# Kernel optimization log

Hardware: AMD Instinct MI355X
Metric: run time of the kernel (lower is better)

The kernel has to match this reference:

```python
import jax, jax.numpy as jnp
import numpy as np
import math

NUM_HEADS = 16
D_MODEL = 1024
B, T = 1, 4096


def setup_inputs() -> dict:
    key = jax.random.key(0)
    kx, kq, kk, kv, ko = jax.random.split(key, 5)
    s = 1.0 / math.sqrt(D_MODEL)
    return {
        "x": jax.random.normal(kx, (B, T, D_MODEL), dtype=jnp.float32),
        "Wq": jax.random.normal(kq, (D_MODEL, D_MODEL), dtype=jnp.float32) * s,
        "Wk": jax.random.normal(kk, (D_MODEL, D_MODEL), dtype=jnp.float32) * s,
        "Wv": jax.random.normal(kv, (D_MODEL, D_MODEL), dtype=jnp.float32) * s,
        "Wo": jax.random.normal(ko, (D_MODEL, D_MODEL), dtype=jnp.float32) * s,
    }


def reference(x, Wq, Wk, Wv, Wo):
    # x: (B, T, D); weights stored torch-Linear style: y = x @ W.T
    Bx, Tx, D = x.shape
    H = NUM_HEADS
    dk = D // H
    q = (x @ Wq.T).reshape(Bx, Tx, H, dk)  # (B,T,H,dk)
    k = (x @ Wk.T).reshape(Bx, Tx, H, dk)
    v = (x @ Wv.T).reshape(Bx, Tx, H, dk)
    # scores: (B,H,T,T), scaled dot-product
    scores = jnp.einsum("bthd,bshd->bhts", q, k) / math.sqrt(dk)
    causal_mask = jnp.triu(jnp.ones((Tx, Tx), dtype=bool), k=1)  # True above diag
    scores = jnp.where(causal_mask, jnp.float32(-jnp.inf), scores).astype(jnp.float32)
    attn = jax.nn.softmax(scores, axis=-1)  # fp32 softmax, as in the torch module
    out = jnp.einsum("bhts,bshd->bthd", attn, v).reshape(Bx, Tx, D)
    return out @ Wo.T
```

## Files before the change

kernel.cpp:

```cpp
#include <hip/hip_runtime.h>
#include <hip/hip_bf16.h>
#include <math.h>

typedef __attribute__((ext_vector_type(8)))  __bf16 bf16x8;
typedef __attribute__((ext_vector_type(4)))  __bf16 bf16x4;
typedef __attribute__((ext_vector_type(4)))  float  f32x4;
typedef __attribute__((ext_vector_type(16))) float  f32x16;

static constexpr int T_SEQ = 4096;
static constexpr int DM    = 1024;
static constexpr int NH    = 16;
static constexpr float QSCALE = 0.125f * 1.44269504088896340736f;

__device__ __forceinline__ void gload16(const void* g, void* l) {
    __builtin_amdgcn_global_load_lds(
        (const __attribute__((address_space(1))) unsigned int*)g,
        (__attribute__((address_space(3))) unsigned int*)l,
        16, 0, 0);
}

__device__ __forceinline__ unsigned cvtpk_bf16(float a, float b) {
    unsigned r;
    asm("v_cvt_pk_bf16_f32 %0, %1, %2" : "=v"(r) : "v"(a), "v"(b));
    return r;
}
__device__ __forceinline__ void permswap(unsigned& x, unsigned& y) {
    asm("v_permlane32_swap_b32 %0, %1" : "+v"(x), "+v"(y));
}
__device__ __forceinline__ float xhalf_max(float v) {
    union { float f; unsigned u; } a, b;
    a.f = v; b.f = v;
    asm volatile("" : "+v"(b.u));
    permswap(a.u, b.u);
    return fmaxf(a.f, b.f);
}
__device__ __forceinline__ float xhalf_sum(float v) {
    union { float f; unsigned u; } a, b;
    a.f = v; b.f = v;
    asm volatile("" : "+v"(b.u));
    permswap(a.u, b.u);
    return a.f + b.f;
}

__global__ __launch_bounds__(256)
void cvt_bf16(const float* __restrict__ in, __bf16* __restrict__ out, int n4) {
    int i = blockIdx.x * blockDim.x + threadIdx.x;
    if (i >= n4) return;
    float4 v = ((const float4*)in)[i];
    bf16x4 o;
    o[0] = (__bf16)v.x; o[1] = (__bf16)v.y; o[2] = (__bf16)v.z; o[3] = (__bf16)v.w;
    ((bf16x4*)out)[i] = o;
}

__global__ __launch_bounds__(256)
void cvt4_bf16(const float* __restrict__ a0, const float* __restrict__ a1,
               const float* __restrict__ a2, const float* __restrict__ a3,
               __bf16* __restrict__ o0, __bf16* __restrict__ o1,
               __bf16* __restrict__ o2, __bf16* __restrict__ o3, int n4) {
    int i = blockIdx.x * blockDim.x + threadIdx.x;
    if (i >= n4) return;
    const float* in = blockIdx.y == 0 ? a0 : blockIdx.y == 1 ? a1 : blockIdx.y == 2 ? a2 : a3;
    __bf16* out     = blockIdx.y == 0 ? o0 : blockIdx.y == 1 ? o1 : blockIdx.y == 2 ? o2 : o3;
    float4 v = ((const float4*)in)[i];
    bf16x4 o;
    o[0] = (__bf16)v.x; o[1] = (__bf16)v.y; o[2] = (__bf16)v.z; o[3] = (__bf16)v.w;
    ((bf16x4*)out)[i] = o;
}

template<bool OUT_BF16>
__device__ __forceinline__ void gemm_body(const __bf16* __restrict__ A,
                                          const __bf16* __restrict__ B,
                                          void* __restrict__ Cout,
                                          int N, int K, float scale,
                                          int bx, int by) {
    __shared__ __align__(16) __bf16 Al[128 * 64];
    __shared__ __align__(16) __bf16 Bl[128 * 64];
    const int tid  = threadIdx.x;
    const int lane = tid & 63;
    const int wid  = tid >> 6;
    const int wr   = wid >> 1, wc = wid & 1;
    const int m0   = by * 128, n0 = bx * 128;
    const int r    = lane & 15, g = lane >> 4;

    f32x4 acc[4][4];
    const f32x4 z4 = {0.f, 0.f, 0.f, 0.f};
    #pragma unroll
    for (int i = 0; i < 4; ++i)
        #pragma unroll
        for (int j = 0; j < 4; ++j) acc[i][j] = z4;

    for (int kt = 0; kt < K; kt += 64) {
        __syncthreads();
        #pragma unroll
        for (int p = 0; p < 4; ++p) {
            int u    = p * 256 + tid;
            int row  = u >> 3;
            int col8 = (u & 7) ^ (row & 7);
            gload16(A + (size_t)(m0 + row) * K + kt + col8 * 8,
                    (char*)Al + (p * 256 + wid * 64) * 16);
            gload16(B + (size_t)(n0 + row) * K + kt + col8 * 8,
                    (char*)Bl + (p * 256 + wid * 64) * 16);
        }
        __syncthreads();
        __builtin_amdgcn_s_setprio(1);
        #pragma unroll
        for (int kk = 0; kk < 2; ++kk) {
            bf16x8 af[4], bfr[4];
            #pragma unroll
            for (int mi = 0; mi < 4; ++mi)
                af[mi] = *(const bf16x8*)&Al[(wr * 64 + mi * 16 + r) * 64 + (((kk * 4 + g) ^ (r & 7)) * 8)];
            #pragma unroll
            for (int nj = 0; nj < 4; ++nj)
                bfr[nj] = *(const bf16x8*)&Bl[(wc * 64 + nj * 16 + r) * 64 + (((kk * 4 + g) ^ (r & 7)) * 8)];
            #pragma unroll
            for (int mi = 0; mi < 4; ++mi)
                #pragma unroll
                for (int nj = 0; nj < 4; ++nj)
                    acc[mi][nj] = __builtin_amdgcn_mfma_f32_16x16x32_bf16(af[mi], bfr[nj], acc[mi][nj], 0, 0, 0);
        }
        __builtin_amdgcn_s_setprio(0);
    }
    #pragma unroll
    for (int mi = 0; mi < 4; ++mi)
        #pragma unroll
        for (int nj = 0; nj < 4; ++nj)
            #pragma unroll
            for (int j = 0; j < 4; ++j) {
                int row = m0 + wr * 64 + mi * 16 + g * 4 + j;
                int col = n0 + wc * 64 + nj * 16 + r;
                float v = acc[mi][nj][j] * scale;
                if (OUT_BF16) ((__bf16*)Cout)[(size_t)row * N + col] = (__bf16)v;
                else          ((float*)Cout)[(size_t)row * N + col]  = v;
            }
}

__global__ __launch_bounds__(256)
void gemm_qkv(const __bf16* __restrict__ A,
              const __bf16* __restrict__ W0, const __bf16* __restrict__ W1,
              const __bf16* __restrict__ W2,
              __bf16* __restrict__ O0, __bf16* __restrict__ O1, __bf16* __restrict__ O2) {
    const int z = blockIdx.z;
    const __bf16* B = z == 0 ? W0 : (z == 1 ? W1 : W2);
    __bf16*       C = z == 0 ? O0 : (z == 1 ? O1 : O2);
    float scale = z == 0 ? QSCALE : 1.0f;
    gemm_body<true>(A, B, C, DM, DM, scale, blockIdx.x, blockIdx.y);
}

__global__ __launch_bounds__(256)
void gemm_out(const __bf16* __restrict__ A, const __bf16* __restrict__ B,
              float* __restrict__ C) {
    gemm_body<false>(A, B, C, DM, DM, 1.0f, blockIdx.x, blockIdx.y);
}

__global__ __launch_bounds__(256)
void vtrans(const __bf16* __restrict__ V, __bf16* __restrict__ Vt) {
    __shared__ __bf16 tl[64][72];
    const int tid = threadIdx.x;
    const int t0  = blockIdx.x * 64;
    const int h   = blockIdx.y;
    #pragma unroll
    for (int p = 0; p < 2; ++p) {
        int c = p * 256 + tid, row = c >> 3, col8 = c & 7;
        *(bf16x8*)&tl[row][col8 * 8] =
            *(const bf16x8*)(V + (size_t)(t0 + row) * DM + h * 64 + col8 * 8);
    }
    __syncthreads();
    #pragma unroll
    for (int p = 0; p < 2; ++p) {
        int c = p * 256 + tid, d = c >> 3, tc8 = c & 7;
        bf16x8 o;
        #pragma unroll
        for (int e = 0; e < 8; ++e) o[e] = tl[tc8 * 8 + e][d];
        *(bf16x8*)(Vt + (size_t)(h * 64 + d) * T_SEQ + t0 + tc8 * 8) = o;
    }
}

__global__ __launch_bounds__(128)
void attn_fwd(const __bf16* __restrict__ Q, const __bf16* __restrict__ Kp,
              const __bf16* __restrict__ Vt, __bf16* __restrict__ O)
{
    __shared__ __align__(16) __bf16 Kl[2][64 * 64];
    __shared__ __align__(16) __bf16 Vl[2][64 * 64];
    const int tid  = threadIdx.x;
    const int lane = tid & 63, wid = tid >> 6;
    const int l31  = lane & 31;
    const int hi   = lane >> 5;
    const int h    = blockIdx.x;
    const int u_   = blockIdx.y & 15, j_ = blockIdx.y >> 4;
    const int qb   = j_ == 0 ? u_ : j_ == 1 ? 31 - u_ : j_ == 2 ? 32 + u_ : 63 - u_;
    const int qw   = qb * 64 + wid * 32;
    const int qg   = qw + l31;

    bf16x8 qf[4];
    #pragma unroll
    for (int kd0 = 0; kd0 < 4; ++kd0)
        qf[kd0] = *(const bf16x8*)(Q + (size_t)qg * DM + h * 64 + kd0 * 16 + hi * 8);

    float m_i = -1e30f, l_i = 0.f;
    f32x16 oacc[2];
    #pragma unroll
    for (int d = 0; d < 2; ++d)
        #pragma unroll
        for (int e = 0; e < 16; ++e) oacc[d][e] = 0.f;

    const int nt = qb + 1;

    auto stage_lds = [&](int t, int buf) {
        #pragma unroll
        for (int p = 0; p < 4; ++p) {
            int u    = p * 128 + tid;
            int row  = u >> 3;
            int col8 = (u & 7) ^ (row & 7);
            gload16(Kp + (size_t)(t * 64 + row) * DM + h * 64 + col8 * 8,
                    (char*)&Kl[buf][0] + (p * 128 + wid * 64) * 16);
            gload16(Vt + (size_t)(h * 64 + row) * T_SEQ + t * 64 + col8 * 8,
                    (char*)&Vl[buf][0] + (p * 128 + wid * 64) * 16);
        }
    };
    stage_lds(0, 0);
    if (nt > 1) stage_lds(1, 1);
    __syncthreads();

    auto qk = [&](f32x16* sdst, int buf) {
        #pragma unroll
        for (int ksub = 0; ksub < 2; ++ksub) {
            const int row = ksub * 32 + l31;
            f32x16 a;
            #pragma unroll
            for (int e = 0; e < 16; ++e) a[e] = 0.f;
            #pragma unroll
            for (int kd0 = 0; kd0 < 4; ++kd0) {
                bf16x8 kf = *(const bf16x8*)
                    &Kl[buf][(row << 6) + ((((kd0 << 1) + hi) ^ (row & 7)) << 3)];
                a = __builtin_amdgcn_mfma_f32_32x32x16_bf16(kf, qf[kd0], a, 0, 0, 0);
            }
            sdst[ksub] = a;
        }
    };
    auto mask_sf = [&](f32x16* s, int t) {
        const int kb = (t << 6) + 4 * hi;
        #pragma unroll
        for (int ksub = 0; ksub < 2; ++ksub)
            #pragma unroll
            for (int e = 0; e < 16; ++e) {
                int k = kb + ksub * 32 + ((e & 3) + 8 * (e >> 2));
                if (k > qg) s[ksub][e] = -1e30f;
            }
    };

    f32x16 sf[2], sfn[2];
    qk(sf, 0);
    if (qb == 0) mask_sf(sf, 0);

    bf16x8 kreg[4], vreg[4];
    for (int t = 0; t < nt; ++t) {
        const int cur = t & 1;
        const bool have_next  = (t + 1 < nt);
        const bool have_next2 = (t + 2 < nt);
        if (have_next2) {
            const int t2 = t + 2;
            #pragma unroll
            for (int p = 0; p < 4; ++p) {
                int u   = p * 128 + tid;
                int row = u >> 3;
                int c   = u & 7;
                kreg[p] = *(const bf16x8*)(Kp + (size_t)(t2 * 64 + row) * DM + h * 64 + c * 8);
                vreg[p] = *(const bf16x8*)(Vt + (size_t)(h * 64 + row) * T_SEQ + t2 * 64 + c * 8);
            }
        }
        __builtin_amdgcn_s_setprio(1);
        if (have_next) {
            qk(sfn, cur ^ 1);
            if (t + 1 == qb) mask_sf(sfn, t + 1);
        }
        __builtin_amdgcn_s_setprio(0);
        float pm;
        {
            float t0[8];
            #pragma unroll
            for (int e = 0; e < 8; ++e)
                t0[e] = fmaxf(fmaxf(sf[0][e], sf[0][e + 8]), fmaxf(sf[1][e], sf[1][e + 8]));
            #pragma unroll
            for (int s = 4; s > 0; s >>= 1)
                #pragma unroll
                for (int e = 0; e < s; ++e) t0[e] = fmaxf(t0[e], t0[e + s]);
            pm = xhalf_max(t0[0]);
        }
        if (pm > m_i + 8.f) {
            float al = exp2f(m_i - pm);
            m_i = pm;
            l_i *= al;
            #pragma unroll
            for (int d = 0; d < 2; ++d)
                #pragma unroll
                for (int e = 0; e < 16; ++e) oacc[d][e] *= al;
        }
        float p[32];
        #pragma unroll
        for (int i = 0; i < 32; ++i)
            p[i] = exp2f(sf[i >> 4][i & 15] - m_i);
        {
            float s0[8];
            #pragma unroll
            for (int e = 0; e < 8; ++e)
                s0[e] = (p[e] + p[e + 8]) + (p[e + 16] + p[e + 24]);
            #pragma unroll
            for (int s = 4; s > 0; s >>= 1)
                #pragma unroll
                for (int e = 0; e < s; ++e) s0[e] += s0[e + s];
            l_i += xhalf_sum(s0[0]);
        }
        __builtin_amdgcn_s_setprio(1);
        #pragma unroll
        for (int ks = 0; ks < 4; ++ks) {
            unsigned w0 = cvtpk_bf16(p[8 * ks + 0], p[8 * ks + 1]);
            unsigned w1 = cvtpk_bf16(p[8 * ks + 2], p[8 * ks + 3]);
            unsigned w2 = cvtpk_bf16(p[8 * ks + 4], p[8 * ks + 5]);
            unsigned w3 = cvtpk_bf16(p[8 * ks + 6], p[8 * ks + 7]);
            permswap(w0, w2);
            permswap(w1, w3);
            union { unsigned u[4]; bf16x8 v; } pu;
            pu.u[0] = w0; pu.u[1] = w1; pu.u[2] = w2; pu.u[3] = w3;
            #pragma unroll
            for (int dsub = 0; dsub < 2; ++dsub) {
                const int row = dsub * 32 + l31;
                bf16x8 vt = *(const bf16x8*)
                    &Vl[cur][(row << 6) + ((((ks << 1) + hi) ^ (row & 7)) << 3)];
                oacc[dsub] = __builtin_amdgcn_mfma_f32_32x32x16_bf16(vt, pu.v, oacc[dsub], 0, 0, 0);
            }
        }
        __builtin_amdgcn_s_setprio(0);
        if (have_next2) {
            __syncthreads();
            #pragma unroll
            for (int p = 0; p < 4; ++p) {
                int u   = p * 128 + tid;
                int row = u >> 3;
                int c   = u & 7;
                *(bf16x8*)&Kl[cur][(row << 6) + ((c ^ (row & 7)) << 3)] = kreg[p];
                *(bf16x8*)&Vl[cur][(row << 6) + ((c ^ (row & 7)) << 3)] = vreg[p];
            }
            __syncthreads();
        }
        if (have_next) {
            sf[0] = sfn[0];
            sf[1] = sfn[1];
        }
    }
    __syncthreads();
    __bf16* ow = &Kl[0][0] + wid * 2048;
    const float invl = 1.f / l_i;
    #pragma unroll
    for (int dsub = 0; dsub < 2; ++dsub)
        #pragma unroll
        for (int e = 0; e < 16; ++e) {
            int d = dsub * 32 + ((e & 3) + 8 * (e >> 2)) + 4 * hi;
            float v = oacc[dsub][e] * invl;
            int bo = l31 * 128 + ((2 * d) ^ ((l31 & 7) << 4));
            *(__bf16*)((char*)ow + bo) = (__bf16)v;
        }
    #pragma unroll
    for (int i = 0; i < 4; ++i) {
        int u  = hi * 4 + i;
        int bo = l31 * 128 + ((u * 16) ^ ((l31 & 7) << 4));
        bf16x8 v8 = *(const bf16x8*)((char*)ow + bo);
        *(bf16x8*)(O + (size_t)qg * DM + h * 64 + u * 8) = v8;
    }
}

extern "C" void kernel_launch(void* const* d_in, const int* in_sizes, int n_in,
                              void* d_out, int out_size, void* d_ws, size_t ws_size,
                              hipStream_t stream) {
    const float* x  = (const float*)d_in[0];
    const float* Wq = (const float*)d_in[1];
    const float* Wk = (const float*)d_in[2];
    const float* Wv = (const float*)d_in[3];
    const float* Wo = (const float*)d_in[4];
    float* out = (float*)d_out;

    char* ws = (char*)d_ws;
    const size_t MB = (size_t)1 << 20;
    __bf16* xb    = (__bf16*)(ws + 0 * MB);
    __bf16* VtG   = (__bf16*)(ws + 0 * MB);
    __bf16* wqb   = (__bf16*)(ws + 8 * MB);
    __bf16* wkb   = (__bf16*)(ws + 10 * MB);
    __bf16* wvb   = (__bf16*)(ws + 12 * MB);
    __bf16* wob   = (__bf16*)(ws + 14 * MB);
    __bf16* Qb    = (__bf16*)(ws + 16 * MB);
    __bf16* Kb    = (__bf16*)(ws + 24 * MB);
    __bf16* Vb    = (__bf16*)(ws + 32 * MB);
    __bf16* attnb = (__bf16*)(ws + 40 * MB);

    const int nX = T_SEQ * DM / 4;
    const int nW = DM * DM / 4;
    cvt_bf16<<<(nX + 255) / 256, 256, 0, stream>>>(x, xb, nX);
    cvt4_bf16<<<dim3((nW + 255) / 256, 4), 256, 0, stream>>>(Wq, Wk, Wv, Wo,
                                                             wqb, wkb, wvb, wob, nW);

    gemm_qkv<<<dim3(DM / 128, T_SEQ / 128, 3), 256, 0, stream>>>(xb, wqb, wkb, wvb, Qb, Kb, Vb);

    vtrans<<<dim3(T_SEQ / 64, NH), 256, 0, stream>>>(Vb, VtG);

    attn_fwd<<<dim3(NH, 64), 128, 0, stream>>>(Qb, Kb, VtG, attnb);

    gemm_out<<<dim3(DM / 128, T_SEQ / 128), 256, 0, stream>>>(attnb, wob, out);
}
```

Baseline: 189.9 us.

## Split long causal query blocks across two KV chunks and combine partial softmax

Query blocks at or beyond index 34 have their KV range split in half and run as two separate workgroups. Each writes unnormalized bf16 partial outputs plus running max and sum, and a new combine kernel merges them into the final attention output. This shortens the longest-running workgroups and reorders blocks longest-first to reduce tail imbalance. The cost is an extra kernel launch, extra global traffic for the partials, and bf16 rounding of the unnormalized partial outputs.

```diff
diff --git a/kernel.cpp b/kernel.cpp
--- a/kernel.cpp
+++ b/kernel.cpp
@@ -10,6 +10,8 @@
 static constexpr int T_SEQ = 4096;
 static constexpr int DM    = 1024;
 static constexpr int NH    = 16;
+static constexpr int SPLIT_QB   = 34;
+static constexpr int SPLIT_ROWS = T_SEQ - SPLIT_QB * 64;
 static constexpr float QSCALE = 0.125f * 1.44269504088896340736f;
 
 __device__ __forceinline__ void gload16(const void* g, void* l) {
@@ -177,7 +179,8 @@
 
 __global__ __launch_bounds__(128)
 void attn_fwd(const __bf16* __restrict__ Q, const __bf16* __restrict__ Kp,
-              const __bf16* __restrict__ Vt, __bf16* __restrict__ O)
+              const __bf16* __restrict__ Vt, __bf16* __restrict__ O,
+              __bf16* __restrict__ U, float* __restrict__ Ml)
 {
     __shared__ __align__(16) __bf16 Kl[2][64 * 64];
     __shared__ __align__(16) __bf16 Vl[2][64 * 64];
@@ -186,10 +189,21 @@
     const int l31  = lane & 31;
     const int hi   = lane >> 5;
     const int h    = blockIdx.x;
-    const int u_   = blockIdx.y & 15, j_ = blockIdx.y >> 4;
-    const int qb   = j_ == 0 ? u_ : j_ == 1 ? 31 - u_ : j_ == 2 ? 32 + u_ : 63 - u_;
-    const int qw   = qb * 64 + wid * 32;
-    const int qg   = qw + l31;
+    const int y    = blockIdx.y;
+    int qb, t0i, t1i, chunk;
+    bool split;
+    if (y < SPLIT_QB) {
+        qb = (SPLIT_QB - 1) - y; t0i = 0; t1i = qb; split = false; chunk = 0;
+    } else {
+        int s = y - SPLIT_QB;
+        qb = 63 - (s >> 1);
+        int n = qb + 1, c0 = n - (n >> 1);
+        split = true;
+        if ((s & 1) == 0) { chunk = 0; t0i = 0;  t1i = c0 - 1; }
+        else              { chunk = 1; t0i = c0; t1i = qb;     }
+    }
+    const int qw = qb * 64 + wid * 32;
+    const int qg = qw + l31;
 
     bf16x8 qf[4];
     #pragma unroll
@@ -202,8 +216,6 @@
     for (int d = 0; d < 2; ++d)
         #pragma unroll
         for (int e = 0; e < 16; ++e) oacc[d][e] = 0.f;
-
-    const int nt = qb + 1;
 
     auto stage_lds = [&](int t, int buf) {
         #pragma unroll
@@ -217,8 +229,8 @@
                     (char*)&Vl[buf][0] + (p * 128 + wid * 64) * 16);
         }
     };
-    stage_lds(0, 0);
-    if (nt > 1) stage_lds(1, 1);
+    stage_lds(t0i, 0);
+    if (t1i > t0i) stage_lds(t0i + 1, 1);
     __syncthreads();
 
     auto qk = [&](f32x16* sdst, int buf) {
@@ -250,13 +262,13 @@
 
     f32x16 sf[2], sfn[2];
     qk(sf, 0);
-    if (qb == 0) mask_sf(sf, 0);
+    if (t0i == qb) mask_sf(sf, t0i);
 
     bf16x8 kreg[4], vreg[4];
-    for (int t = 0; t < nt; ++t) {
-        const int cur = t & 1;
-        const bool have_next  = (t + 1 < nt);
-        const bool have_next2 = (t + 2 < nt);
+    for (int t = t0i; t <= t1i; ++t) {
+        const int cur = (t - t0i) & 1;
+        const bool have_next  = (t + 1 <= t1i);
+        const bool have_next2 = (t + 2 <= t1i);
         if (have_next2) {
             const int t2 = t + 2;
             #pragma unroll
@@ -349,7 +361,7 @@
     }
     __syncthreads();
     __bf16* ow = &Kl[0][0] + wid * 2048;
-    const float invl = 1.f / l_i;
+    const float invl = split ? 1.0f : (1.f / l_i);
     #pragma unroll
     for (int dsub = 0; dsub < 2; ++dsub)
         #pragma unroll
@@ -359,13 +371,51 @@
             int bo = l31 * 128 + ((2 * d) ^ ((l31 & 7) << 4));
             *(__bf16*)((char*)ow + bo) = (__bf16)v;
         }
-    #pragma unroll
-    for (int i = 0; i < 4; ++i) {
-        int u  = hi * 4 + i;
-        int bo = l31 * 128 + ((u * 16) ^ ((l31 & 7) << 4));
-        bf16x8 v8 = *(const bf16x8*)((char*)ow + bo);
-        *(bf16x8*)(O + (size_t)qg * DM + h * 64 + u * 8) = v8;
-    }
+    if (!split) {
+        #pragma unroll
+        for (int i = 0; i < 4; ++i) {
+            int u  = hi * 4 + i;
+            int bo = l31 * 128 + ((u * 16) ^ ((l31 & 7) << 4));
+            bf16x8 v8 = *(const bf16x8*)((char*)ow + bo);
+            *(bf16x8*)(O + (size_t)qg * DM + h * 64 + u * 8) = v8;
+        }
+    } else {
+        const int ridx = qg - SPLIT_QB * 64;
+        #pragma unroll
+        for (int i = 0; i < 4; ++i) {
+            int u  = hi * 4 + i;
+            int bo = l31 * 128 + ((u * 16) ^ ((l31 & 7) << 4));
+            bf16x8 v8 = *(const bf16x8*)((char*)ow + bo);
+            *(bf16x8*)(U + ((size_t)(chunk * NH + h) * SPLIT_ROWS + ridx) * 64 + u * 8) = v8;
+        }
+        if (hi == 0) {
+            float* mlp = Ml + ((size_t)(chunk * NH + h) * SPLIT_ROWS + ridx) * 2;
+            mlp[0] = m_i;
+            mlp[1] = l_i;
+        }
+    }
+}
+
+__global__ __launch_bounds__(256)
+void attn_combine(const __bf16* __restrict__ U, const float* __restrict__ Ml,
+                  __bf16* __restrict__ O) {
+    int gid = blockIdx.x * 256 + threadIdx.x;
+    int rh  = gid >> 3;
+    int e8  = gid & 7;
+    int ridx = rh >> 4, h = rh & 15;
+    const float* ml0 = Ml + ((size_t)(0 * NH + h) * SPLIT_ROWS + ridx) * 2;
+    const float* ml1 = Ml + ((size_t)(1 * NH + h) * SPLIT_ROWS + ridx) * 2;
+    float m0 = ml0[0], l0 = ml0[1], m1 = ml1[0], l1 = ml1[1];
+    float M  = fmaxf(m0, m1);
+    float s0 = exp2f(m0 - M), s1 = exp2f(m1 - M);
+    float inv = 1.f / (l0 * s0 + l1 * s1);
+    bf16x8 u0 = *(const bf16x8*)(U + ((size_t)(0 * NH + h) * SPLIT_ROWS + ridx) * 64 + e8 * 8);
+    bf16x8 u1 = *(const bf16x8*)(U + ((size_t)(1 * NH + h) * SPLIT_ROWS + ridx) * 64 + e8 * 8);
+    bf16x8 o;
+    #pragma unroll
+    for (int j = 0; j < 8; ++j)
+        o[j] = (__bf16)(((float)u0[j] * s0 + (float)u1[j] * s1) * inv);
+    *(bf16x8*)(O + (size_t)(SPLIT_QB * 64 + ridx) * DM + h * 64 + e8 * 8) = o;
 }
 
 extern "C" void kernel_launch(void* const* d_in, const int* in_sizes, int n_in,
@@ -383,12 +433,14 @@
     __bf16* xb    = (__bf16*)(ws + 0 * MB);
     __bf16* VtG   = (__bf16*)(ws + 0 * MB);
     __bf16* wqb   = (__bf16*)(ws + 8 * MB);
+    float*  MlB   = (float*)(ws + 8 * MB);
     __bf16* wkb   = (__bf16*)(ws + 10 * MB);
     __bf16* wvb   = (__bf16*)(ws + 12 * MB);
     __bf16* wob   = (__bf16*)(ws + 14 * MB);
     __bf16* Qb    = (__bf16*)(ws + 16 * MB);
     __bf16* Kb    = (__bf16*)(ws + 24 * MB);
     __bf16* Vb    = (__bf16*)(ws + 32 * MB);
+    __bf16* UB    = (__bf16*)(ws + 32 * MB);
     __bf16* attnb = (__bf16*)(ws + 40 * MB);
 
     const int nX = T_SEQ * DM / 4;
@@ -401,7 +453,10 @@
 
     vtrans<<<dim3(T_SEQ / 64, NH), 256, 0, stream>>>(Vb, VtG);
 
-    attn_fwd<<<dim3(NH, 64), 128, 0, stream>>>(Qb, Kb, VtG, attnb);
+    attn_fwd<<<dim3(NH, SPLIT_QB + 2 * (64 - SPLIT_QB)), 128, 0, stream>>>(
+        Qb, Kb, VtG, attnb, UB, MlB);
+
+    attn_combine<<<(SPLIT_ROWS * NH * 8) / 256, 256, 0, stream>>>(UB, MlB, attnb);
 
     gemm_out<<<dim3(DM / 128, T_SEQ / 128), 256, 0, stream>>>(attnb, wob, out);
 }
```

Measured after the change: 165.2 us. -13.0%, faster.
